# Kernel tuning notes

Hardware: AMD Instinct MI355X
Metric: run time of the kernel (lower is better)

The kernel has to match this reference:

```python
import jax, jax.numpy as jnp
import numpy as np

NJ, NS = 30000, 12000            # num job / skill nodes
E_JS, E_SJ, E_SS = 300000, 300000, 150000
SBERT, HID, OUT = 384, 128, 128
H = 2                             # GAT heads (concat=True)
NEG_SLOPE = 0.2


def setup_inputs() -> dict:
    key = jax.random.key(0)
    ks = iter(jax.random.split(key, 64))
    nrm = lambda shape, s=1.0: jax.random.normal(next(ks), shape, jnp.float32) * s
    ridx = lambda n, hi: jax.random.randint(next(ks), (n,), 0, hi, jnp.int32)
    W = 0.05  # weight scale to keep activations sane across layers
    return dict(
        x_job=nrm((NJ, SBERT)), x_skill=nrm((NS, SBERT)),
        ei_js_src=ridx(E_JS, NJ), ei_js_dst=ridx(E_JS, NS),
        ei_sj_src=ridx(E_SJ, NS), ei_sj_dst=ridx(E_SJ, NJ),
        ei_ss_src=ridx(E_SS, NS), ei_ss_dst=ridx(E_SS, NS),
        query=nrm((SBERT,)),
        W0_job=nrm((SBERT, HID), W), b0_job=jnp.zeros((HID,), jnp.float32),
        g0_job=jnp.ones((HID,), jnp.float32), be0_job=jnp.zeros((HID,), jnp.float32),
        W0_skill=nrm((SBERT, HID), W), b0_skill=jnp.zeros((HID,), jnp.float32),
        g0_skill=jnp.ones((HID,), jnp.float32), be0_skill=jnp.zeros((HID,), jnp.float32),
        gat_Ws=nrm((2, 3, HID, H * HID), W), gat_Wd=nrm((2, 3, HID, H * HID), W),
        gat_as=nrm((2, 3, H, HID), W), gat_ad=nrm((2, 3, H, HID), W),
        gat_b=jnp.zeros((2, 3, H * HID), jnp.float32),
        inter_W=nrm((2, 2, H * HID, HID), W), inter_b=jnp.zeros((2, 2, HID), jnp.float32),
        Wjf=nrm((HID, OUT), W), bjf=jnp.zeros((OUT,), jnp.float32),
        Wq=nrm((SBERT, OUT), W), bq=jnp.zeros((OUT,), jnp.float32),
    )


def _layer_norm(x, g, b):
    mu = x.mean(-1, keepdims=True)
    var = ((x - mu) ** 2).mean(-1, keepdims=True)
    return (x - mu) * jax.lax.rsqrt(var + 1e-5) * g + b


def _gat(x_src, x_dst, src, dst, Ws, Wd, a_s, a_d, bias, num_dst):
    # PyG GATConv: lin_src/lin_dst (no bias), additive attention, scatter-softmax over dst.
    hs = (x_src @ Ws).reshape(-1, H, HID)            # [Ns,H,C]
    hd = (x_dst @ Wd).reshape(-1, H, HID)            # [Nd,H,C]
    e = jax.nn.leaky_relu((hs * a_s).sum(-1)[src] + (hd * a_d).sum(-1)[dst], NEG_SLOPE)  # [E,H]
    m = jax.ops.segment_max(e, dst, num_segments=num_dst)
    p = jnp.exp(e - m[dst])
    den = jax.ops.segment_sum(p, dst, num_segments=num_dst)
    w = p / (den[dst] + 1e-16)                       # [E,H]
    out = jax.ops.segment_sum(hs[src] * w[:, :, None], dst, num_segments=num_dst)
    return out.reshape(num_dst, H * HID) + bias


def _forward(x_job, x_skill, query,
             W0_job, b0_job, g0_job, be0_job, W0_skill, b0_skill, g0_skill, be0_skill,
             gat_Ws, gat_Wd, gat_as, gat_ad, gat_b, inter_W, inter_b, Wjf, bjf, Wq, bq,
             ei_js_src, ei_js_dst, ei_sj_src, ei_sj_dst, ei_ss_src, ei_ss_dst):
    # initial per-type lin + LN + relu (dropout = identity in eval)
    xj = jax.nn.relu(_layer_norm(x_job @ W0_job + b0_job, g0_job, be0_job))
    xs = jax.nn.relu(_layer_norm(x_skill @ W0_skill + b0_skill, g0_skill, be0_skill))
    # skill->skill relation adds self loops (src == dst node type)
    loops = jnp.arange(NS, dtype=jnp.int32)
    ss_src = jnp.concatenate([ei_ss_src, loops])
    ss_dst = jnp.concatenate([ei_ss_dst, loops])
    for i in range(2):  # num_layers
        o_s = (_gat(xj, xs, ei_js_src, ei_js_dst, gat_Ws[i, 0], gat_Wd[i, 0],
                    gat_as[i, 0], gat_ad[i, 0], gat_b[i, 0], NS)
               + _gat(xs, xs, ss_src, ss_dst, gat_Ws[i, 2], gat_Wd[i, 2],
                      gat_as[i, 2], gat_ad[i, 2], gat_b[i, 2], NS))  # HeteroConv aggr='sum'
        o_j = _gat(xs, xj, ei_sj_src, ei_sj_dst, gat_Ws[i, 1], gat_Wd[i, 1],
                   gat_as[i, 1], gat_ad[i, 1], gat_b[i, 1], NJ)
        xj = jax.nn.relu(o_j @ inter_W[i, 0] + inter_b[i, 0])
        xs = jax.nn.relu(o_s @ inter_W[i, 1] + inter_b[i, 1])
    job_emb = xj @ Wjf + bjf                          # [NJ,OUT]
    q = query @ Wq + bq                               # [OUT]
    scores = job_emb @ q                              # [NJ]
    return scores, job_emb, q


def reference(x_job, x_skill, ei_js_src, ei_js_dst, ei_sj_src, ei_sj_dst,
              ei_ss_src, ei_ss_dst, query,
              W0_job, b0_job, g0_job, be0_job, W0_skill, b0_skill, g0_skill, be0_skill,
              gat_Ws, gat_Wd, gat_as, gat_ad, gat_b, inter_W, inter_b,
              Wjf, bjf, Wq, bq):
    return _forward(x_job, x_skill, query,
                    W0_job, b0_job, g0_job, be0_job, W0_skill, b0_skill, g0_skill, be0_skill,
                    gat_Ws, gat_Wd, gat_as, gat_ad, gat_b, inter_W, inter_b, Wjf, bjf, Wq, bq,
                    ei_js_src, ei_js_dst, ei_sj_src, ei_sj_dst, ei_ss_src, ei_ss_dst)
```

## Files before the change

kernel.cpp:

```cpp
#include <hip/hip_runtime.h>
#include <hip/hip_bf16.h>
#include <math.h>

#define NJ 30000
#define NS 12000
#define E_JS 300000
#define E_SJ 300000
#define E_SS 150000
#define ETOT (E_JS + E_SJ + E_SS + NS)
#define NBINS (NS + NJ + NS)
#define NBUK ((NBINS + 63) / 64)
#define SBERT 384
#define HIST_NB 512
#define SCAT_NB 480
#define CAST_MATS 14
#define CAST_BPM 48
#define PREP_CAST (CAST_MATS * CAST_BPM)
#define PREP_WA   (PREP_CAST + 12)
#define PREP_QV   PREP_WA
#define PREP_GB   (PREP_QV + 1)
#define PREP_HIST (PREP_GB + 1)

static inline int cdiv(int a, int b) { return (a + b - 1) / b; }

typedef __attribute__((ext_vector_type(8))) short bf8_t;
typedef __attribute__((ext_vector_type(4))) float f4_t;
typedef unsigned short u16;

__device__ inline float bf2f(unsigned short u) {
    union { unsigned int i; float f; } z; z.i = ((unsigned int)u) << 16; return z.f;
}
__device__ inline unsigned short f2bf(float f) {
    unsigned int x = __float_as_uint(f);
    unsigned int r = (x + 0x7fffu + ((x >> 16) & 1u)) >> 16;
    return (unsigned short)r;
}

__device__ inline void edge_decode(int e, const int* js_src, const int* js_dst,
                                   const int* sj_src, const int* sj_dst,
                                   const int* ss_src, const int* ss_dst,
                                   int& src, int& bin) {
    if (e < E_JS) { src = js_src[e]; bin = js_dst[e]; }
    else if (e < E_JS + E_SJ) { int i = e - E_JS; src = sj_src[i]; bin = NS + sj_dst[i]; }
    else if (e < E_JS + E_SJ + E_SS) { int i = e - E_JS - E_SJ; src = ss_src[i]; bin = NS + NJ + ss_dst[i]; }
    else { int i = e - E_JS - E_SJ - E_SS; src = i; bin = NS + NJ + i; }
}

struct CastT { const float* src; unsigned short* dst; int K; int N; int srcLd; int dstLd; };
struct PrepArgs {
    CastT m[CAST_MATS];
    const float* Ws; const float* as_; const float* Wd; const float* ad_;
    float* wsa; float* wda; int* bcnt;
    const float* query; const float* Wq; const float* bq; float* qv;
    const float* gat_b; float* gbS;
    const int* js_src; const int* js_dst;
    const int* sj_src; const int* sj_dst;
    const int* ss_src; const int* ss_dst;
};

__global__ __launch_bounds__(256) void k_prep(PrepArgs A) {
    __shared__ float ldt[32][33];
    __shared__ int lh[NBUK];
    int b = blockIdx.x;
    if (b < PREP_CAST) {
        int mi = b / CAST_BPM, bx = b % CAST_BPM;
        CastT cm = A.m[mi];
        int tilesN = cm.N >> 5;
        int total = (cm.K >> 5) * tilesN;
        if (bx >= total) return;
        int tk = bx / tilesN, tn = bx % tilesN;
        int k0 = tk * 32, n0 = tn * 32;
        int col = threadIdx.x & 31;
        int row0 = threadIdx.x >> 5;
#pragma unroll
        for (int r = 0; r < 4; ++r) {
            int kk = row0 + r * 8;
            ldt[kk][col] = cm.src[(size_t)(k0 + kk) * cm.srcLd + n0 + col];
        }
        __syncthreads();
#pragma unroll
        for (int r = 0; r < 4; ++r) {
            int nn = row0 + r * 8;
            cm.dst[(size_t)(n0 + nn) * cm.dstLd + k0 + col] = f2bf(ldt[col][nn]);
        }
    } else if (b < PREP_WA) {
        int id = (b - PREP_CAST) * 256 + threadIdx.x;
        if (id >= 2 * 1536) return;
        int which = id / 1536;
        int r = id % 1536;
        int lr = r / 256;
        int kh = r % 256;
        int k = kh / 2, h = kh % 2;
        const float* W = which ? A.Wd : A.Ws;
        const float* a = which ? A.ad_ : A.as_;
        const float* wrow = W + ((size_t)(lr * 128 + k)) * 256 + h * 128;
        const float* arow = a + (size_t)(lr * 2 + h) * 128;
        float acc = 0.f;
        for (int c2 = 0; c2 < 128; ++c2) acc += wrow[c2] * arow[c2];
        (which ? A.wda : A.wsa)[lr * 256 + k * 2 + h] = acc;
    } else if (b == PREP_QV) {
        int c = threadIdx.x;
        if (c < 128) {
            float acc = A.bq[c];
            for (int k = 0; k < SBERT; ++k) acc += A.query[k] * A.Wq[(size_t)k * 128 + c];
            A.qv[c] = acc;
        }
    } else if (b == PREP_GB) {
        int c = threadIdx.x;
        if (c < 256) A.gbS[c] = A.gat_b[c] + A.gat_b[512 + c];
    } else {
        int t = threadIdx.x;
        for (int i = t; i < NBUK; i += 256) lh[i] = 0;
        __syncthreads();
        int hb = b - PREP_HIST;
        for (int e = hb * 256 + t; e < ETOT; e += HIST_NB * 256) {
            int src, bin;
            edge_decode(e, A.js_src, A.js_dst, A.sj_src, A.sj_dst, A.ss_src, A.ss_dst, src, bin);
            atomicAdd(&lh[bin >> 6], 1);
        }
        __syncthreads();
        for (int i = t; i < NBUK; i += 256) {
            int v = lh[i];
            if (v) atomicAdd(&A.bcnt[i], v);
        }
    }
}

struct GJob {
    const void* X; const unsigned short* Wt;
    const float* bias; const float* gamma; const float* beta;
    void* Y; int M; int K; int N; int ldY; int srcf32;
    const float* qv; float* sc;
    int aMode = 0;
    const float* wav0 = nullptr; const float* wav1 = nullptr;
    const float* wav2 = nullptr; const float* wav3 = nullptr;
    float* aOut = nullptr; int aStride = 0;
};
struct GPair { GJob a; GJob b; int blocksA; };

template <int EPI>
__device__ void mgemm_body(const GPair& P, int bx) {
    int mb = bx;
    GJob g = (mb < P.blocksA) ? P.a : P.b;
    if (mb >= P.blocksA) mb -= P.blocksA;
    const int row0 = mb * 64;

    __shared__ __align__(16) float As[2][64][32];
    __shared__ __align__(16) unsigned short Bs[2][128][32];
    const int t = threadIdx.x;
    const int wave = t >> 6, lane = t & 63;
    const int q = lane >> 4, c = lane & 15;
    const int K = g.K;
    const float* Xf = (const float*)g.X;

    f4_t acc[8];
#pragma unroll
    for (int nt = 0; nt < 8; ++nt) acc[nt] = (f4_t){0.f, 0.f, 0.f, 0.f};

    auto STAGE = [&](int cur, int k0) {
#pragma unroll
        for (int i = 0; i < 2; ++i) {
            int bi = i * 256 + t;
            int row = bi >> 3, b = bi & 7;
            int ra = row0 + row; ra = (ra < g.M) ? ra : (g.M - 1);
            const float* gsrc = Xf + (size_t)ra * K + k0 + ((b ^ (row & 7)) << 2);
            __builtin_amdgcn_global_load_lds(
                (__attribute__((address_space(1))) void*)gsrc,
                (__attribute__((address_space(3))) void*)((char*)&As[cur][0][0] + ((i * 4 + wave) << 10)),
                16, 0, 0);
        }
#pragma unroll
        for (int i = 0; i < 2; ++i) {
            int bi = i * 256 + t;
            int row = bi >> 2, b = bi & 3;
            const unsigned short* gsrc = g.Wt + (size_t)row * K + k0 + ((b ^ ((row >> 1) & 3)) << 3);
            __builtin_amdgcn_global_load_lds(
                (__attribute__((address_space(1))) void*)gsrc,
                (__attribute__((address_space(3))) void*)((char*)&Bs[cur][0][0] + ((i * 4 + wave) << 10)),
                16, 0, 0);
        }
    };

    auto MF = [&](int cur) {
        const char* Ab = (const char*)&As[cur][0][0];
        const char* Bb = (const char*)&Bs[cur][0][0];
        int r = wave * 16 + c;
        int sw = r & 7;
        f4_t fa0 = *(const f4_t*)(Ab + r * 128 + (((q * 2) ^ sw) << 4));
        f4_t fa1 = *(const f4_t*)(Ab + r * 128 + (((q * 2 + 1) ^ sw) << 4));
        bf8_t af;
        af[0] = (short)f2bf(fa0[0]); af[1] = (short)f2bf(fa0[1]);
        af[2] = (short)f2bf(fa0[2]); af[3] = (short)f2bf(fa0[3]);
        af[4] = (short)f2bf(fa1[0]); af[5] = (short)f2bf(fa1[1]);
        af[6] = (short)f2bf(fa1[2]); af[7] = (short)f2bf(fa1[3]);
#pragma unroll
        for (int nt = 0; nt < 8; ++nt) {
            int rb = nt * 16 + c;
            bf8_t bfr = *(const bf8_t*)(Bb + rb * 64 + ((q ^ ((rb >> 1) & 3)) << 4));
            acc[nt] = __builtin_amdgcn_mfma_f32_16x16x32_bf16(af, bfr, acc[nt], 0, 0, 0);
        }
    };

    STAGE(0, 0);
    int cur = 0;
    for (int k0 = 0; k0 < K; k0 += 32) {
        asm volatile("s_waitcnt vmcnt(0)" ::: "memory");
        __syncthreads();
        if (k0 + 32 < K) STAGE(cur ^ 1, k0 + 32);
        MF(cur);
        cur ^= 1;
    }

    float bcol[8], gcol[8], becol[8];
#pragma unroll
    for (int nt = 0; nt < 8; ++nt) {
        bcol[nt] = g.bias[nt * 16 + c];
        if constexpr (EPI == 3) {
            gcol[nt] = g.gamma[nt * 16 + c];
            becol[nt] = g.beta[nt * 16 + c];
        }
    }

#pragma unroll
    for (int r = 0; r < 4; ++r) {
        int grow = row0 + wave * 16 + q * 4 + r;
        float v[8];
#pragma unroll
        for (int nt = 0; nt < 8; ++nt) v[nt] = acc[nt][r] + bcol[nt];
        if constexpr (EPI == 3) {
            float s = 0.f, ss = 0.f;
#pragma unroll
            for (int nt = 0; nt < 8; ++nt) { s += v[nt]; ss += v[nt] * v[nt]; }
#pragma unroll
            for (int m = 8; m >= 1; m >>= 1) {
                s += __shfl_xor(s, m, 64);
                ss += __shfl_xor(ss, m, 64);
            }
            float mu = s * (1.f / 128.f);
            float var = ss * (1.f / 128.f) - mu * mu;
            float rs = rsqrtf(var + 1e-5f);
#pragma unroll
            for (int nt = 0; nt < 8; ++nt)
                v[nt] = fmaxf((v[nt] - mu) * rs * gcol[nt] + becol[nt], 0.f);
        }
        if (g.aMode > 0) {
            float pa[8];
#pragma unroll
            for (int i = 0; i < 8; ++i) pa[i] = 0.f;
#pragma unroll
            for (int nt = 0; nt < 8; ++nt) {
                int col = nt * 16 + c;
                float2 w0 = *(const float2*)&g.wav0[col * 2];
                pa[0] += v[nt] * w0.x; pa[1] += v[nt] * w0.y;
                if (g.aMode > 1) {
                    float2 w1 = *(const float2*)&g.wav1[col * 2];
                    pa[2] += v[nt] * w1.x; pa[3] += v[nt] * w1.y;
                }
                if (g.aMode > 2) {
                    float2 w2 = *(const float2*)&g.wav2[col * 2];
                    float2 w3 = *(const float2*)&g.wav3[col * 2];
                    pa[4] += v[nt] * w2.x; pa[5] += v[nt] * w2.y;
                    pa[6] += v[nt] * w3.x; pa[7] += v[nt] * w3.y;
                }
            }
#pragma unroll
            for (int m = 8; m >= 1; m >>= 1) {
                pa[0] += __shfl_xor(pa[0], m, 64); pa[1] += __shfl_xor(pa[1], m, 64);
                pa[2] += __shfl_xor(pa[2], m, 64); pa[3] += __shfl_xor(pa[3], m, 64);
                pa[4] += __shfl_xor(pa[4], m, 64); pa[5] += __shfl_xor(pa[5], m, 64);
                pa[6] += __shfl_xor(pa[6], m, 64); pa[7] += __shfl_xor(pa[7], m, 64);
            }
            if (c == 0 && grow < g.M) {
                float* ao = &g.aOut[(size_t)grow * g.aStride];
                ao[0] = pa[0]; ao[1] = pa[1];
                if (g.aMode > 1) { ao[2] = pa[2]; ao[3] = pa[3]; }
                if (g.aMode > 2) { ao[4] = pa[4]; ao[5] = pa[5]; ao[6] = pa[6]; ao[7] = pa[7]; }
            }
        }
        if (grow < g.M) {
            unsigned short* Y = (unsigned short*)g.Y;
#pragma unroll
            for (int nt = 0; nt < 8; ++nt)
                Y[(size_t)grow * g.ldY + nt * 16 + c] = f2bf(v[nt]);
        }
    }
}

__global__ __launch_bounds__(256) void k_scan(
    const int* __restrict__ bcnt, int* __restrict__ bukoff, int* __restrict__ bukcur) {
    __shared__ int sd[256];
    int t = threadIdx.x;
    int i0 = t * 4;
    int v0 = (i0 < NBUK) ? bcnt[i0] : 0;
    int v1 = (i0 + 1 < NBUK) ? bcnt[i0 + 1] : 0;
    int v2 = (i0 + 2 < NBUK) ? bcnt[i0 + 2] : 0;
    int v3 = (i0 + 3 < NBUK) ? bcnt[i0 + 3] : 0;
    int csum = v0 + v1 + v2 + v3;
    sd[t] = csum;
    __syncthreads();
    for (int off = 1; off < 256; off <<= 1) {
        int tmp = (t >= off) ? sd[t - off] : 0;
        __syncthreads();
        sd[t] += tmp;
        __syncthreads();
    }
    int excl = sd[t] - csum;
    int p0 = excl, p1 = excl + v0, p2 = excl + v0 + v1, p3 = excl + v0 + v1 + v2;
    if (i0 < NBUK) { bukoff[i0] = p0; bukcur[i0] = p0; }
    if (i0 + 1 < NBUK) { bukoff[i0 + 1] = p1; bukcur[i0 + 1] = p1; }
    if (i0 + 2 < NBUK) { bukoff[i0 + 2] = p2; bukcur[i0 + 2] = p2; }
    if (i0 + 3 < NBUK) { bukoff[i0 + 3] = p3; bukcur[i0 + 3] = p3; }
    if (t == 0) bukoff[NBUK] = ETOT;
}

__global__ __launch_bounds__(256) void k_lin0_scat(
    GPair P, int gemmBlocks,
    const int* __restrict__ js_src, const int* __restrict__ js_dst,
    const int* __restrict__ sj_src, const int* __restrict__ sj_dst,
    const int* __restrict__ ss_src, const int* __restrict__ ss_dst,
    int* __restrict__ bukcur, uint2* __restrict__ pairs) {
    if (blockIdx.x < (unsigned)gemmBlocks) {
        mgemm_body<3>(P, blockIdx.x);
        return;
    }
    __shared__ int lh[NBUK];
    __shared__ int lbase[NBUK];
    int t = threadIdx.x;
    int sb = blockIdx.x - gemmBlocks;
    const int CH = (ETOT + SCAT_NB - 1) / SCAT_NB;
    const int beg = sb * CH;
    const int endi = (beg + CH < ETOT) ? beg + CH : ETOT;
    if (beg >= ETOT) return;
    for (int i = t; i < NBUK; i += 256) lh[i] = 0;
    __syncthreads();
    for (int e = beg + t; e < endi; e += 256) {
        int src, bin;
        edge_decode(e, js_src, js_dst, sj_src, sj_dst, ss_src, ss_dst, src, bin);
        atomicAdd(&lh[bin >> 6], 1);
    }
    __syncthreads();
    for (int i = t; i < NBUK; i += 256) {
        int v = lh[i];
        lbase[i] = v ? atomicAdd(&bukcur[i], v) : 0;
    }
    __syncthreads();
    for (int i = t; i < NBUK; i += 256) lh[i] = 0;
    __syncthreads();
    for (int e = beg + t; e < endi; e += 256) {
        int src, bin;
        edge_decode(e, js_src, js_dst, sj_src, sj_dst, ss_src, ss_dst, src, bin);
        int bu = bin >> 6;
        int pos = lbase[bu] + atomicAdd(&lh[bu], 1);
        pairs[pos] = make_uint2((unsigned)src, (unsigned)bin);
    }
}

__global__ __launch_bounds__(256) void k_finalize(
    const uint2* __restrict__ pairs, const int* __restrict__ bukoff,
    int* __restrict__ offs, int* __restrict__ esrc) {
    int b = blockIdx.x, t = threadIdx.x;
    int base = bukoff[b], endi = bukoff[b + 1];
    __shared__ int cnt[64], excl[64], curs[64];
    if (t < 64) cnt[t] = 0;
    __syncthreads();
    for (int i = base + t; i < endi; i += 256)
        atomicAdd(&cnt[pairs[i].y & 63], 1);
    __syncthreads();
    if (t < 64) {
        int v = cnt[t];
        int inc = v;
#pragma unroll
        for (int off = 1; off < 64; off <<= 1) {
            int tmp = __shfl_up(inc, off, 64);
            if (t >= off) inc += tmp;
        }
        excl[t] = inc - v;
        curs[t] = inc - v;
    }
    __syncthreads();
    for (int i = base + t; i < endi; i += 256) {
        uint2 p = pairs[i];
        int lb = p.y & 63;
        int pos = atomicAdd(&curs[lb], 1);
        esrc[base + pos] = (int)p.x;
    }
    if (t < 64) {
        int bin = b * 64 + t;
        if (bin < NBINS) offs[bin] = base + excl[t];
    }
    if (b == 0 && t == 0) offs[NBINS] = ETOT;
}

__device__ inline void fm8(float p0, float p1, uint4 u, float a0[8], float a1[8]) {
    float x0 = __uint_as_float(u.x << 16);
    float x1 = __uint_as_float(u.x & 0xffff0000u);
    float x2 = __uint_as_float(u.y << 16);
    float x3 = __uint_as_float(u.y & 0xffff0000u);
    float x4 = __uint_as_float(u.z << 16);
    float x5 = __uint_as_float(u.z & 0xffff0000u);
    float x6 = __uint_as_float(u.w << 16);
    float x7 = __uint_as_float(u.w & 0xffff0000u);
    a0[0] += p0 * x0; a0[1] += p0 * x1; a0[2] += p0 * x2; a0[3] += p0 * x3;
    a0[4] += p0 * x4; a0[5] += p0 * x5; a0[6] += p0 * x6; a0[7] += p0 * x7;
    a1[0] += p1 * x0; a1[1] += p1 * x1; a1[2] += p1 * x2; a1[3] += p1 * x3;
    a1[4] += p1 * x4; a1[5] += p1 * x5; a1[6] += p1 * x6; a1[7] += p1 * x7;
}

__device__ inline void rel_run(
    const int* __restrict__ esrc, int beg, int end,
    const float* __restrict__ aSrc, int aShift, int aOff, float adx, float ady,
    const unsigned short* __restrict__ rows, int colOff, int g,
    float a0[8], float a1[8], float& den0, float& den1) {
    int j = beg;
    for (; j + 8 <= end; j += 8) {
        int s0 = esrc[j + g];
        int s1 = esrc[j + 4 + g];
        uint4 u0 = *(const uint4*)&rows[(unsigned)s0 * 128 + colOff];
        uint4 u1 = *(const uint4*)&rows[(unsigned)s1 * 128 + colOff];
        float2 f0 = *(const float2*)&aSrc[((unsigned)s0 << aShift) + aOff];
        float2 f1 = *(const float2*)&aSrc[((unsigned)s1 << aShift) + aOff];
        float e00 = f0.x + adx; e00 = e00 > 0.f ? e00 : 0.2f * e00;
        float e01 = f0.y + ady; e01 = e01 > 0.f ? e01 : 0.2f * e01;
        float e10 = f1.x + adx; e10 = e10 > 0.f ? e10 : 0.2f * e10;
        float e11 = f1.y + ady; e11 = e11 > 0.f ? e11 : 0.2f * e11;
        float p00 = __expf(e00), p01 = __expf(e01);
        float p10 = __expf(e10), p11 = __expf(e11);
        fm8(p00, p01, u0, a0, a1);
        fm8(p10, p11, u1, a0, a1);
        den0 += p00 + p10; den1 += p01 + p11;
    }
    for (; j < end; j += 4) {
        int e = j + g;
        bool ok = e < end;
        int s = esrc[ok ? e : j];
        uint4 u = *(const uint4*)&rows[(unsigned)s * 128 + colOff];
        float2 f = *(const float2*)&aSrc[((unsigned)s << aShift) + aOff];
        float e0 = f.x + adx; e0 = e0 > 0.f ? e0 : 0.2f * e0;
        float e1 = f.y + ady; e1 = e1 > 0.f ? e1 : 0.2f * e1;
        float p0 = ok ? __expf(e0) : 0.f;
        float p1 = ok ? __expf(e1) : 0.f;
        fm8(p0, p1, u, a0, a1);
        den0 += p0; den1 += p1;
    }
}

__device__ inline void store8(unsigned short* dst, const float v[8]) {
    uint4 o;
    o.x = (unsigned)f2bf(v[0]) | ((unsigned)f2bf(v[1]) << 16);
    o.y = (unsigned)f2bf(v[2]) | ((unsigned)f2bf(v[3]) << 16);
    o.z = (unsigned)f2bf(v[4]) | ((unsigned)f2bf(v[5]) << 16);
    o.w = (unsigned)f2bf(v[6]) | ((unsigned)f2bf(v[7]) << 16);
    *(uint4*)dst = o;
}

__device__ inline void finish_store(float a0[8], float a1[8], float den0, float den1,
                                    int lane, unsigned short* base) {
    float d0 = den0; d0 += __shfl_xor(d0, 16, 64); d0 += __shfl_xor(d0, 32, 64);
    float d1 = den1; d1 += __shfl_xor(d1, 16, 64); d1 += __shfl_xor(d1, 32, 64);
    float s0 = 1.f / (d0 + 1e-16f), s1 = 1.f / (d1 + 1e-16f);
    float o0[8], o1[8];
#pragma unroll
    for (int i = 0; i < 8; ++i) {
        float t0 = a0[i]; t0 += __shfl_xor(t0, 16, 64); t0 += __shfl_xor(t0, 32, 64);
        float t1 = a1[i]; t1 += __shfl_xor(t1, 16, 64); t1 += __shfl_xor(t1, 32, 64);
        o0[i] = t0 * s0; o1[i] = t1 * s1;
    }
    if ((lane >> 4) == 0) {
        store8(base, o0);
        store8(base + 128, o1);
    }
}

__global__ __launch_bounds__(256) void k_gather_all(
    const int* __restrict__ offs, const int* __restrict__ esrc,
    const float* __restrict__ aJ, const float* __restrict__ aS,
    const unsigned short* __restrict__ rowsJ,
    const unsigned short* __restrict__ rowsS,
    unsigned short* __restrict__ aggS,
    unsigned short* __restrict__ aggJ,
    int jobOnly) {
    int wave = threadIdx.x >> 6, lane = threadIdx.x & 63;
    int idx = blockIdx.x * 4 + wave;
    int g = lane >> 4, cl = lane & 15;
    int colOff = cl * 8;

    float a0[8], a1[8], den0, den1;

    if (jobOnly) {
        if (idx >= NJ) return;
        int d = idx;
#pragma unroll
        for (int i = 0; i < 8; ++i) { a0[i] = 0.f; a1[i] = 0.f; }
        den0 = den1 = 0.f;
        int bb = NS + d;
        float2 ad = *(const float2*)&aJ[(unsigned)d * 4 + 2];
        rel_run(esrc, offs[bb], offs[bb + 1], aS, 3, 4, ad.x, ad.y, rowsS, colOff, g, a0, a1, den0, den1);
        finish_store(a0, a1, den0, den1, lane, &aggJ[(size_t)d * 256 + colOff]);
        return;
    }
    if (idx < NS) {
        int d = idx;
#pragma unroll
        for (int i = 0; i < 8; ++i) { a0[i] = 0.f; a1[i] = 0.f; }
        den0 = den1 = 0.f;
        float2 adA = *(const float2*)&aS[(unsigned)d * 8 + 2];
        rel_run(esrc, offs[d], offs[d + 1], aJ, 2, 0, adA.x, adA.y, rowsJ, colOff, g, a0, a1, den0, den1);
        finish_store(a0, a1, den0, den1, lane, &aggS[(size_t)d * 512 + colOff]);
#pragma unroll
        for (int i = 0; i < 8; ++i) { a0[i] = 0.f; a1[i] = 0.f; }
        den0 = den1 = 0.f;
        int bb = NS + NJ + d;
        float2 adB = *(const float2*)&aS[(unsigned)d * 8 + 6];
        rel_run(esrc, offs[bb], offs[bb + 1], aS, 3, 0, adB.x, adB.y, rowsS, colOff, g, a0, a1, den0, den1);
        finish_store(a0, a1, den0, den1, lane, &aggS[(size_t)d * 512 + 256 + colOff]);
    } else if (idx < NS + NJ) {
        int d = idx - NS;
#pragma unroll
        for (int i = 0; i < 8; ++i) { a0[i] = 0.f; a1[i] = 0.f; }
        den0 = den1 = 0.f;
        int bb = NS + d;
        float2 ad = *(const float2*)&aJ[(unsigned)d * 4 + 2];
        rel_run(esrc, offs[bb], offs[bb + 1], aS, 3, 4, ad.x, ad.y, rowsS, colOff, g, a0, a1, den0, den1);
        finish_store(a0, a1, den0, den1, lane, &aggJ[(size_t)d * 256 + colOff]);
    }
}

struct FJob {
    const unsigned short* X; int K1; int M;
    const unsigned short* Wt1; const float* bias1;
    const unsigned short* Wt2; const float* bias2;
    const float* wa; float* aOut; int aStride;
    unsigned short* Y2;
};
struct FPair { FJob a; FJob b; int blocksA; };

__global__ __launch_bounds__(256) void k_fused2(FPair P) {
    int mb = blockIdx.x;
    FJob g = (mb < P.blocksA) ? P.a : P.b;
    if (mb >= P.blocksA) mb -= P.blocksA;
    const int row0 = mb * 64;
    const int K1 = g.K1;

    __shared__ __align__(16) unsigned short Al[64][40];
    __shared__ __align__(16) unsigned short Bl[128][40];
    __shared__ __align__(16) unsigned short Y1l[4][64][40];
    const int t = threadIdx.x;
    const int wave = t >> 6, lane = t & 63;
    const int q = lane >> 4, c = lane & 15;

    f4_t acc2[8];
#pragma unroll
    for (int nt = 0; nt < 8; ++nt) acc2[nt] = (f4_t){0.f, 0.f, 0.f, 0.f};

    for (int np = 0; np < 2; ++np) {
        f4_t acc[8];
#pragma unroll
        for (int nt = 0; nt < 8; ++nt) acc[nt] = (f4_t){0.f, 0.f, 0.f, 0.f};
        for (int k0 = 0; k0 < K1; k0 += 32) {
#pragma unroll
            for (int it = 0; it < 3; ++it) {
                int idx = t + it * 256;
                int r = idx >> 2, cc = (idx & 3) * 8;
                if (r < 64) {
                    int gr = row0 + r;
                    uint4 va = (gr < g.M) ? *(const uint4*)&g.X[(size_t)gr * K1 + k0 + cc]
                                          : make_uint4(0u, 0u, 0u, 0u);
                    *(uint4*)&Al[r][cc] = va;
                } else {
                    int br = r - 64;
                    *(uint4*)&Bl[br][cc] = *(const uint4*)&g.Wt1[(size_t)(np * 128 + br) * K1 + k0 + cc];
                }
            }
            __syncthreads();
            bf8_t af = *(const bf8_t*)&Al[wave * 16 + c][q * 8];
#pragma unroll
            for (int nt = 0; nt < 8; ++nt) {
                bf8_t bfr = *(const bf8_t*)&Bl[nt * 16 + c][q * 8];
                acc[nt] = __builtin_amdgcn_mfma_f32_16x16x32_bf16(af, bfr, acc[nt], 0, 0, 0);
            }
            __syncthreads();
        }
        float bcol[8];
#pragma unroll
        for (int nt = 0; nt < 8; ++nt) bcol[nt] = g.bias1[np * 128 + nt * 16 + c];
#pragma unroll
        for (int r = 0; r < 4; ++r) {
            int row = wave * 16 + q * 4 + r;
#pragma unroll
            for (int nt = 0; nt < 8; ++nt)
                Y1l[nt >> 1][row][(nt & 1) * 16 + c] = f2bf(acc[nt][r] + bcol[nt]);
        }
        __syncthreads();
        for (int k0 = 0; k0 < 128; k0 += 32) {
#pragma unroll
            for (int it = 0; it < 2; ++it) {
                int idx = t + it * 256;
                int br = idx >> 2, cc = (idx & 3) * 8;
                *(uint4*)&Bl[br][cc] = *(const uint4*)&g.Wt2[(size_t)br * 256 + np * 128 + k0 + cc];
            }
            __syncthreads();
            bf8_t af = *(const bf8_t*)&Y1l[k0 >> 5][wave * 16 + c][q * 8];
#pragma unroll
            for (int nt = 0; nt < 8; ++nt) {
                bf8_t bfr = *(const bf8_t*)&Bl[nt * 16 + c][q * 8];
                acc2[nt] = __builtin_amdgcn_mfma_f32_16x16x32_bf16(af, bfr, acc2[nt], 0, 0, 0);
            }
            __syncthreads();
        }
    }

    float b2[8];
#pragma unroll
    for (int nt = 0; nt < 8; ++nt) b2[nt] = g.bias2[nt * 16 + c];
#pragma unroll
    for (int r = 0; r < 4; ++r) {
        int grow = row0 + wave * 16 + q * 4 + r;
        float v[8];
#pragma unroll
        for (int nt = 0; nt < 8; ++nt) v[nt] = fmaxf(acc2[nt][r] + b2[nt], 0.f);
        if (g.wa) {
            float pa0 = 0.f, pa1 = 0.f;
#pragma unroll
            for (int nt = 0; nt < 8; ++nt) {
                float2 w0 = *(const float2*)&g.wa[(nt * 16 + c) * 2];
                pa0 += v[nt] * w0.x; pa1 += v[nt] * w0.y;
            }
#pragma unroll
            for (int m = 8; m >= 1; m >>= 1) {
                pa0 += __shfl_xor(pa0, m, 64);
                pa1 += __shfl_xor(pa1, m, 64);
            }
            if (c == 0 && grow < g.M) {
                g.aOut[(size_t)grow * g.aStride + 0] = pa0;
                g.aOut[(size_t)grow * g.aStride + 1] = pa1;
            }
        }
        if (g.Y2 && grow < g.M) {
#pragma unroll
            for (int nt = 0; nt < 8; ++nt)
                g.Y2[(size_t)grow * 128 + nt * 16 + c] = f2bf(v[nt]);
        }
    }
}

struct F3 {
    const unsigned short* X; int M;
    const unsigned short* Wt1; const float* bias1;
    const unsigned short* Wt2; const float* bias2;
    const unsigned short* Wt3; const float* bias3;
    const float* qv; float* sc; float* Y;
};

__global__ __launch_bounds__(256) void k_fused3(F3 g) {
    int mb = blockIdx.x;
    const int row0 = mb * 64;
    __shared__ __align__(16) unsigned short Al[64][40];
    __shared__ __align__(16) unsigned short Bl[128][40];
    __shared__ __align__(16) unsigned short Yl[4][64][40];
    const int t = threadIdx.x;
    const int wave = t >> 6, lane = t & 63;
    const int q = lane >> 4, c = lane & 15;

    f4_t acc2[8];
#pragma unroll
    for (int nt = 0; nt < 8; ++nt) acc2[nt] = (f4_t){0.f, 0.f, 0.f, 0.f};

    for (int np = 0; np < 2; ++np) {
        f4_t acc[8];
#pragma unroll
        for (int nt = 0; nt < 8; ++nt) acc[nt] = (f4_t){0.f, 0.f, 0.f, 0.f};
        for (int k0 = 0; k0 < 256; k0 += 32) {
#pragma unroll
            for (int it = 0; it < 3; ++it) {
                int idx = t + it * 256;
                int r = idx >> 2, cc = (idx & 3) * 8;
                if (r < 64) {
                    int gr = row0 + r;
                    uint4 va = (gr < g.M) ? *(const uint4*)&g.X[(size_t)gr * 256 + k0 + cc]
                                          : make_uint4(0u, 0u, 0u, 0u);
                    *(uint4*)&Al[r][cc] = va;
                } else {
                    int br = r - 64;
                    *(uint4*)&Bl[br][cc] = *(const uint4*)&g.Wt1[(size_t)(np * 128 + br) * 256 + k0 + cc];
                }
            }
            __syncthreads();
            bf8_t af = *(const bf8_t*)&Al[wave * 16 + c][q * 8];
#pragma unroll
            for (int nt = 0; nt < 8; ++nt) {
                bf8_t bfr = *(const bf8_t*)&Bl[nt * 16 + c][q * 8];
                acc[nt] = __builtin_amdgcn_mfma_f32_16x16x32_bf16(af, bfr, acc[nt], 0, 0, 0);
            }
            __syncthreads();
        }
        float bcol[8];
#pragma unroll
        for (int nt = 0; nt < 8; ++nt) bcol[nt] = g.bias1[np * 128 + nt * 16 + c];
#pragma unroll
        for (int r = 0; r < 4; ++r) {
            int row = wave * 16 + q * 4 + r;
#pragma unroll
            for (int nt = 0; nt < 8; ++nt)
                Yl[nt >> 1][row][(nt & 1) * 16 + c] = f2bf(acc[nt][r] + bcol[nt]);
        }
        __syncthreads();
        for (int k0 = 0; k0 < 128; k0 += 32) {
#pragma unroll
            for (int it = 0; it < 2; ++it) {
                int idx = t + it * 256;
                int br = idx >> 2, cc = (idx & 3) * 8;
                *(uint4*)&Bl[br][cc] = *(const uint4*)&g.Wt2[(size_t)br * 256 + np * 128 + k0 + cc];
            }
            __syncthreads();
            bf8_t af = *(const bf8_t*)&Yl[k0 >> 5][wave * 16 + c][q * 8];
#pragma unroll
            for (int nt = 0; nt < 8; ++nt) {
                bf8_t bfr = *(const bf8_t*)&Bl[nt * 16 + c][q * 8];
                acc2[nt] = __builtin_amdgcn_mfma_f32_16x16x32_bf16(af, bfr, acc2[nt], 0, 0, 0);
            }
            __syncthreads();
        }
    }

    {
        float b2[8];
#pragma unroll
        for (int nt = 0; nt < 8; ++nt) b2[nt] = g.bias2[nt * 16 + c];
#pragma unroll
        for (int r = 0; r < 4; ++r) {
            int row = wave * 16 + q * 4 + r;
#pragma unroll
            for (int nt = 0; nt < 8; ++nt)
                Yl[nt >> 1][row][(nt & 1) * 16 + c] = f2bf(fmaxf(acc2[nt][r] + b2[nt], 0.f));
        }
        __syncthreads();
    }

    f4_t acc3[8];
#pragma unroll
    for (int nt = 0; nt < 8; ++nt) acc3[nt] = (f4_t){0.f, 0.f, 0.f, 0.f};
    for (int k0 = 0; k0 < 128; k0 += 32) {
#pragma unroll
        for (int it = 0; it < 2; ++it) {
            int idx = t + it * 256;
            int br = idx >> 2, cc = (idx & 3) * 8;
            *(uint4*)&Bl[br][cc] = *(const uint4*)&g.Wt3[(size_t)br * 128 + k0 + cc];
        }
        __syncthreads();
        bf8_t af = *(const bf8_t*)&Yl[k0 >> 5][wave * 16 + c][q * 8];
#pragma unroll
        for (int nt = 0; nt < 8; ++nt) {
            bf8_t bfr = *(const bf8_t*)&Bl[nt * 16 + c][q * 8];
            acc3[nt] = __builtin_amdgcn_mfma_f32_16x16x32_bf16(af, bfr, acc3[nt], 0, 0, 0);
        }
        __syncthreads();
    }
    float b3[8], qcol[8];
#pragma unroll
    for (int nt = 0; nt < 8; ++nt) {
        b3[nt] = g.bias3[nt * 16 + c];
        qcol[nt] = g.qv[nt * 16 + c];
    }
#pragma unroll
    for (int r = 0; r < 4; ++r) {
        int grow = row0 + wave * 16 + q * 4 + r;
        float v[8];
#pragma unroll
        for (int nt = 0; nt < 8; ++nt) v[nt] = acc3[nt][r] + b3[nt];
        float part = 0.f;
#pragma unroll
        for (int nt = 0; nt < 8; ++nt) part += v[nt] * qcol[nt];
#pragma unroll
        for (int m = 8; m >= 1; m >>= 1) part += __shfl_xor(part, m, 64);
        if (grow < g.M) {
            if (c == 0) g.sc[grow] = part;
#pragma unroll
            for (int nt = 0; nt < 8; ++nt)
                g.Y[(size_t)grow * 128 + nt * 16 + c] = v[nt];
        }
    }
}

extern "C" void kernel_launch(void* const* d_in, const int* in_sizes, int n_in,
                              void* d_out, int out_size, void* d_ws, size_t ws_size,
                              hipStream_t stream) {
    const float* x_job   = (const float*)d_in[0];
    const float* x_skill = (const float*)d_in[1];
    const int* js_src = (const int*)d_in[2];
    const int* js_dst = (const int*)d_in[3];
    const int* sj_src = (const int*)d_in[4];
    const int* sj_dst = (const int*)d_in[5];
    const int* ss_src = (const int*)d_in[6];
    const int* ss_dst = (const int*)d_in[7];
    const float* query    = (const float*)d_in[8];
    const float* W0_job   = (const float*)d_in[9];
    const float* b0_job   = (const float*)d_in[10];
    const float* g0_job   = (const float*)d_in[11];
    const float* be0_job  = (const float*)d_in[12];
    const float* W0_skill = (const float*)d_in[13];
    const float* b0_skill = (const float*)d_in[14];
    const float* g0_skill = (const float*)d_in[15];
    const float* be0_skill= (const float*)d_in[16];
    const float* gat_Ws = (const float*)d_in[17];
    const float* gat_Wd = (const float*)d_in[18];
    const float* gat_as = (const float*)d_in[19];
    const float* gat_ad = (const float*)d_in[20];
    const float* gat_b  = (const float*)d_in[21];
    const float* inter_W = (const float*)d_in[22];
    const float* inter_b = (const float*)d_in[23];
    const float* Wjf = (const float*)d_in[24];
    const float* bjf = (const float*)d_in[25];
    const float* Wq  = (const float*)d_in[26];
    const float* bq  = (const float*)d_in[27];

    char* w = (char*)d_ws;
    auto alloc = [&](size_t bytes) -> void* {
        void* p = (void*)w;
        w += (bytes + 255) & ~(size_t)255;
        return p;
    };
    u16* xj   = (u16*)alloc((size_t)NJ * 128 * 2);
    u16* xs   = (u16*)alloc((size_t)NS * 128 * 2);
    u16* xs1  = (u16*)alloc((size_t)NS * 128 * 2);
    u16* aggJ  = (u16*)alloc((size_t)NJ * 256 * 2);
    u16* aggJ1 = (u16*)alloc((size_t)NJ * 256 * 2);
    u16* aggS  = (u16*)alloc((size_t)NS * 512 * 2);
    u16* WtW0j = (u16*)alloc((size_t)SBERT * 128 * 2);
    u16* WtW0s = (u16*)alloc((size_t)SBERT * 128 * 2);
    u16* WsS1  = (u16*)alloc((size_t)256 * 512 * 2);
    u16* WsJ0  = (u16*)alloc((size_t)256 * 256 * 2);
    u16* WsJ1  = (u16*)alloc((size_t)256 * 256 * 2);
    u16* WtI00 = (u16*)alloc((size_t)128 * 256 * 2);
    u16* WtI01 = (u16*)alloc((size_t)128 * 256 * 2);
    u16* WtI10 = (u16*)alloc((size_t)128 * 256 * 2);
    u16* WtJf  = (u16*)alloc((size_t)128 * 128 * 2);
    float* gbS = (float*)alloc(256 * 4);
    float* aJ = (float*)alloc((size_t)NJ * 4 * 4);
    float* aS = (float*)alloc((size_t)NS * 8 * 4);
    float* wsa = (float*)alloc(6 * 256 * 4);
    float* wda = (float*)alloc(6 * 256 * 4);
    int* bcnt   = (int*)alloc((size_t)NBUK * 4);
    int* bukoff = (int*)alloc((size_t)(NBUK + 1) * 4);
    int* bukcur = (int*)alloc((size_t)NBUK * 4);
    uint2* pairs = (uint2*)alloc((size_t)ETOT * 8);
    int* offs = (int*)alloc((size_t)(NBINS + 1) * 4);
    int* esrc = (int*)alloc((size_t)ETOT * 4);

    float* out = (float*)d_out;
    float* scores  = out;
    float* job_emb = out + NJ;
    float* qv      = out + NJ + (size_t)NJ * 128;

    const int mbJ = cdiv(NJ, 64);
    const int mbS = cdiv(NS, 64);
    const int gemmB = mbJ + mbS;

    hipMemsetAsync(bcnt, 0, (size_t)NBUK * 4, stream);
    hipMemsetAsync(WsS1, 0, (size_t)256 * 512 * 2, stream);
    hipMemsetAsync(WsJ0, 0, (size_t)256 * 256 * 2, stream);
    hipMemsetAsync(WsJ1, 0, (size_t)256 * 256 * 2, stream);

    {
        const size_t WS = (size_t)128 * 256;
        const size_t IW = (size_t)256 * 128;
        PrepArgs A;
        A.m[0]  = {W0_job,   WtW0j, SBERT, 128, 128, SBERT};
        A.m[1]  = {W0_skill, WtW0s, SBERT, 128, 128, SBERT};
        A.m[2]  = {gat_Ws + 0 * WS,       WsS1,                       128, 128, 256, 512};
        A.m[3]  = {gat_Ws + 0 * WS + 128, WsS1 + 128 * 512 + 128,     128, 128, 256, 512};
        A.m[4]  = {gat_Ws + 2 * WS,       WsS1 + 256,                 128, 128, 256, 512};
        A.m[5]  = {gat_Ws + 2 * WS + 128, WsS1 + 128 * 512 + 384,     128, 128, 256, 512};
        A.m[6]  = {gat_Ws + 1 * WS,       WsJ0,                       128, 128, 256, 256};
        A.m[7]  = {gat_Ws + 1 * WS + 128, WsJ0 + 128 * 256 + 128,     128, 128, 256, 256};
        A.m[8]  = {gat_Ws + 4 * WS,       WsJ1,                       128, 128, 256, 256};
        A.m[9]  = {gat_Ws + 4 * WS + 128, WsJ1 + 128 * 256 + 128,     128, 128, 256, 256};
        A.m[10] = {inter_W + 0 * IW, WtI00, 256, 128, 128, 256};
        A.m[11] = {inter_W + 1 * IW, WtI01, 256, 128, 128, 256};
        A.m[12] = {inter_W + 2 * IW, WtI10, 256, 128, 128, 256};
        A.m[13] = {Wjf, WtJf, 128, 128, 128, 128};
        A.Ws = gat_Ws; A.as_ = gat_as; A.Wd = gat_Wd; A.ad_ = gat_ad;
        A.wsa = wsa; A.wda = wda; A.bcnt = bcnt;
        A.query = query; A.Wq = Wq; A.bq = bq; A.qv = qv;
        A.gat_b = gat_b; A.gbS = gbS;
        A.js_src = js_src; A.js_dst = js_dst;
        A.sj_src = sj_src; A.sj_dst = sj_dst;
        A.ss_src = ss_src; A.ss_dst = ss_dst;
        k_prep<<<PREP_HIST + HIST_NB, 256, 0, stream>>>(A);
    }

    k_scan<<<1, 256, 0, stream>>>(bcnt, bukoff, bukcur);

    {
        GPair P;
        P.a = {x_job, WtW0j, b0_job, g0_job, be0_job, xj, NJ, SBERT, 128, 128, 1,
               nullptr, nullptr, 2, wsa + 0, wda + 256, nullptr, nullptr, aJ, 4};
        P.b = {x_skill, WtW0s, b0_skill, g0_skill, be0_skill, xs, NS, SBERT, 128, 128, 1,
               nullptr, nullptr, 4, wsa + 2 * 256, wda + 0, wsa + 1 * 256, wda + 2 * 256, aS, 8};
        P.blocksA = mbJ;
        k_lin0_scat<<<gemmB + SCAT_NB, 256, 0, stream>>>(
            P, gemmB, js_src, js_dst, sj_src, sj_dst, ss_src, ss_dst, bukcur, pairs);
    }

    k_finalize<<<NBUK, 256, 0, stream>>>(pairs, bukoff, offs, esrc);

    k_gather_all<<<cdiv(NS + NJ, 4), 256, 0, stream>>>(
        offs, esrc, aJ, aS, xj, xs, aggS, aggJ, 0);

    {
        FPair P;
        P.a = {aggJ, 256, NJ, WsJ0, gat_b + 256, WtI00, inter_b + 0,
               wda + 4 * 256, aJ + 2, 4, nullptr};
        P.b = {aggS, 512, NS, WsS1, gbS, WtI01, inter_b + 128,
               wsa + 4 * 256, aS + 4, 8, xs1};
        P.blocksA = mbJ;
        k_fused2<<<gemmB, 256, 0, stream>>>(P);
    }

    k_gather_all<<<cdiv(NJ, 4), 256, 0, stream>>>(
        offs, esrc, aJ, aS, nullptr, xs1, nullptr, aggJ1, 1);

    {
        F3 g3;
        g3.X = aggJ1; g3.M = NJ;
        g3.Wt1 = WsJ1; g3.bias1 = gat_b + 4 * 256;
        g3.Wt2 = WtI10; g3.bias2 = inter_b + 2 * 128;
        g3.Wt3 = WtJf; g3.bias3 = bjf;
        g3.qv = qv; g3.sc = scores; g3.Y = job_emb;
        k_fused3<<<mbJ, 256, 0, stream>>>(g3);
    }
}
```

Baseline: 330.4 us.

## Deepen GEMM K-loop to four-stage LDS pipeline and parallelize attention-weight prep

The mgemm K loop moves from a double-buffered LDS pipeline to four buffers with three stages in flight, using partial vmcnt waits so that global-to-LDS loads overlap more MFMA work. The loop is fully unrolled for a fixed 12 iterations, which hardcodes K=384. The prep step that folds the attention vectors into the weights now uses 16 lanes per output, with float4 loads and a shuffle reduction, instead of one serial thread per output. In exchange, the GEMM doubles its LDS footprint, which may reduce occupancy, and it will break for any K other than 384.

```diff
diff --git a/kernel.cpp b/kernel.cpp
--- a/kernel.cpp
+++ b/kernel.cpp
@@ -16,7 +16,7 @@
 #define CAST_MATS 14
 #define CAST_BPM 48
 #define PREP_CAST (CAST_MATS * CAST_BPM)
-#define PREP_WA   (PREP_CAST + 12)
+#define PREP_WA   (PREP_CAST + 192)
 #define PREP_QV   PREP_WA
 #define PREP_GB   (PREP_QV + 1)
 #define PREP_HIST (PREP_GB + 1)
@@ -84,20 +84,28 @@
             cm.dst[(size_t)(n0 + nn) * cm.dstLd + k0 + col] = f2bf(ldt[col][nn]);
         }
     } else if (b < PREP_WA) {
-        int id = (b - PREP_CAST) * 256 + threadIdx.x;
-        if (id >= 2 * 1536) return;
-        int which = id / 1536;
-        int r = id % 1536;
-        int lr = r / 256;
-        int kh = r % 256;
-        int k = kh / 2, h = kh % 2;
-        const float* W = which ? A.Wd : A.Ws;
-        const float* a = which ? A.ad_ : A.as_;
-        const float* wrow = W + ((size_t)(lr * 128 + k)) * 256 + h * 128;
-        const float* arow = a + (size_t)(lr * 2 + h) * 128;
-        float acc = 0.f;
-        for (int c2 = 0; c2 < 128; ++c2) acc += wrow[c2] * arow[c2];
-        (which ? A.wda : A.wsa)[lr * 256 + k * 2 + h] = acc;
+        int qw = ((b - PREP_CAST) * 256 + threadIdx.x) >> 4;
+        int cl = threadIdx.x & 15;
+        if (qw < 2 * 1536) {
+            int which = qw / 1536;
+            int r = qw % 1536;
+            int lr = r / 256;
+            int kh = r % 256;
+            int k = kh / 2, h = kh % 2;
+            const float* W = which ? A.Wd : A.Ws;
+            const float* a = which ? A.ad_ : A.as_;
+            const float* wrow = W + ((size_t)(lr * 128 + k)) * 256 + h * 128 + cl * 8;
+            const float* arow = a + (size_t)(lr * 2 + h) * 128 + cl * 8;
+            float4 w0 = *(const float4*)wrow, w1 = *(const float4*)(wrow + 4);
+            float4 a0 = *(const float4*)arow, a1 = *(const float4*)(arow + 4);
+            float acc = w0.x * a0.x + w0.y * a0.y + w0.z * a0.z + w0.w * a0.w
+                      + w1.x * a1.x + w1.y * a1.y + w1.z * a1.z + w1.w * a1.w;
+            acc += __shfl_xor(acc, 1, 64);
+            acc += __shfl_xor(acc, 2, 64);
+            acc += __shfl_xor(acc, 4, 64);
+            acc += __shfl_xor(acc, 8, 64);
+            if (cl == 0) (which ? A.wda : A.wsa)[lr * 256 + k * 2 + h] = acc;
+        }
     } else if (b == PREP_QV) {
         int c = threadIdx.x;
         if (c < 128) {
@@ -145,8 +153,8 @@
     if (mb >= P.blocksA) mb -= P.blocksA;
     const int row0 = mb * 64;
 
-    __shared__ __align__(16) float As[2][64][32];
-    __shared__ __align__(16) unsigned short Bs[2][128][32];
+    __shared__ __align__(16) float As[4][64][32];
+    __shared__ __align__(16) unsigned short Bs[4][128][32];
     const int t = threadIdx.x;
     const int wave = t >> 6, lane = t & 63;
     const int q = lane >> 4, c = lane & 15;
@@ -202,13 +210,17 @@
     };
 
     STAGE(0, 0);
-    int cur = 0;
-    for (int k0 = 0; k0 < K; k0 += 32) {
-        asm volatile("s_waitcnt vmcnt(0)" ::: "memory");
-        __syncthreads();
-        if (k0 + 32 < K) STAGE(cur ^ 1, k0 + 32);
-        MF(cur);
-        cur ^= 1;
+    STAGE(1, 32);
+    STAGE(2, 64);
+#pragma unroll
+    for (int k = 0; k < 12; ++k) {
+        if (k < 10)      asm volatile("s_waitcnt vmcnt(8)" ::: "memory");
+        else if (k == 10) asm volatile("s_waitcnt vmcnt(4)" ::: "memory");
+        else             asm volatile("s_waitcnt vmcnt(0)" ::: "memory");
+        __builtin_amdgcn_s_barrier();
+        asm volatile("" ::: "memory");
+        if (k + 3 < 12) STAGE((k + 3) & 3, (k + 3) * 32);
+        MF(k & 3);
     }
 
     float bcol[8], gcol[8], becol[8];
```

After: 340.2 us. 3.0% more time.
